# Optimization experiments

Hardware: AMD Instinct MI355X
Metric: run time of the kernel (lower is better)

Reference implementation:

```python
import jax, jax.numpy as jnp
import numpy as np

N_CAMS = 6
N_RAYS = 200
N_UNI = 32
N_G = 4
N_PG = 8
MAX_D = 100.0
SOM_SIG = 2.0
GRID_W = 400
RAW_W, RAW_H = 1600.0, 900.0
SCENE = np.array([-51.2, -51.2, -5.0, 51.2, 51.2, 3.0], dtype=np.float32)
LOSS_W = {'kl': 1.0, 'dist2closest': 0.01, 'color': 1.0, 'reprojection': 1.0}


def _pe(x):
    freqs = jnp.pi * (2.0 ** jnp.arange(6, dtype=x.dtype))
    xb = x[..., None, :] * freqs[:, None]
    flat = lambda t: t.reshape(t.shape[:-2] + (t.shape[-2] * t.shape[-1],))
    return jnp.concatenate([x, flat(jnp.sin(xb)), flat(jnp.cos(xb))], axis=-1)


def _bilinear(img, u, v):
    C, H, W = img.shape
    x0 = jnp.floor(u)
    y0 = jnp.floor(v)
    valid = (u >= 0) & (u <= W - 1) & (v >= 0) & (v <= H - 1)
    x0i = jnp.clip(x0.astype(jnp.int32), 0, W - 1)
    x1i = jnp.clip(x0i + 1, 0, W - 1)
    y0i = jnp.clip(y0.astype(jnp.int32), 0, H - 1)
    y1i = jnp.clip(y0i + 1, 0, H - 1)
    wx = u - x0
    wy = v - y0
    out = (img[:, y0i, x0i] * ((1 - wx) * (1 - wy))[None]
           + img[:, y0i, x1i] * (wx * (1 - wy))[None]
           + img[:, y1i, x0i] * ((1 - wx) * wy)[None]
           + img[:, y1i, x1i] * (wx * wy)[None])
    out = jnp.moveaxis(out, 0, -1) * valid[..., None]
    return out, valid


def _resnet_fc(feat, z, win, bin_, wz, bz, w0, b0, w1, b1, wout, bout):
    x = feat @ win + bin_
    for i in range(wz.shape[0]):
        x = x + z @ wz[i] + bz[i]
        h = jax.nn.relu(x)
        h = jax.nn.relu(h @ w0[i] + b0[i])
        h = h @ w1[i] + b1[i]
        x = x + h
    return jax.nn.relu(x) @ wout + bout


def _forward(cam_feat, bev_feat, source_imgs, target_imgs, raw_cam_Ks, source_cam_Ks,
             lidar2cams, source_cam2input_lidars, source_cam2target_cams,
             mlp_win, mlp_bin, mlp_wz, mlp_bz, mlp_w0, mlp_b0, mlp_w1, mlp_b1, mlp_wout, mlp_bout,
             g_win, g_bin, g_wz, g_bz, g_w0, g_b0, g_w1, g_b1, g_wout, g_bout, pixel_idx):
    cf = cam_feat[0]
    bf = bev_feat[0]
    si = source_imgs[0, 0]
    ti = target_imgs[0, 0]
    rK = raw_cam_Ks[0, :, :3, :3]
    sK = source_cam_Ks[0, 0, :, :3, :3]
    invK = jnp.linalg.inv(sK)
    l2c = lidar2cams[0]
    s2in = source_cam2input_lidars[0, 0]
    s2tg = source_cam2target_cams[0, 0]
    center = jnp.asarray((SCENE[:3] + SCENE[3:]) / 2.0)
    half = jnp.asarray((SCENE[3:] - SCENE[:3]) / 2.0)
    mlp_p = (mlp_win, mlp_bin, mlp_wz, mlp_bz, mlp_w0, mlp_b0, mlp_w1, mlp_b1, mlp_wout, mlp_bout)
    g_p = (g_win, g_bin, g_wz, g_bz, g_w0, g_b0, g_w1, g_b1, g_wout, g_bout)

    def per_cam(cf_c, si_c, ti_c, rK_c, sK_c, invK_c, l2c_c, s2in_c, s2tg_c, idx):
        N = idx.shape[0]
        x = (idx % GRID_W).astype(jnp.float32) * 2.0
        y = (idx // GRID_W).astype(jnp.float32) * 2.0
        pix_h = jnp.stack([x, y, jnp.ones_like(x)], axis=-1)
        dirs = pix_h @ invK_c.T
        d_u = (jnp.arange(N_UNI, dtype=jnp.float32) + 0.5) / N_UNI * MAX_D
        d_u_b = jnp.broadcast_to(d_u, (N, N_UNI))
        Hf, Wf = cf_c.shape[1], cf_c.shape[2]
        Hb, Wb = bf.shape[1], bf.shape[2]

        def eval_pts(d):
            pts_cam = dirs[:, None, :] * d[..., None]
            pts_lid = pts_cam @ s2in_c[:3, :3].T + s2in_c[:3, 3]
            pc = pts_lid @ l2c_c[:3, :3].T + l2c_c[:3, 3]
            z = pc[..., 2]
            zs = jnp.maximum(z, 1e-3)
            uvw = pc @ rK_c.T
            fu = uvw[..., 0] / zs * (Wf / RAW_W)
            fv = uvw[..., 1] / zs * (Hf / RAW_H)
            cam_lat, cval = _bilinear(cf_c, fu, fv)
            cval = cval & (z > 0.1)
            bx = (pts_lid[..., 0] - SCENE[0]) / (SCENE[3] - SCENE[0]) * (Wb - 1)
            by = (pts_lid[..., 1] - SCENE[1]) / (SCENE[4] - SCENE[1]) * (Hb - 1)
            bev_lat, bval = _bilinear(bf, bx, by)
            valid = cval & bval
            latent = jnp.concatenate([bev_lat, cam_lat], axis=-1) * valid[..., None]
            pln = (pts_lid - center) / half
            pcn = pts_cam / MAX_D
            vd = dirs / jnp.linalg.norm(dirs, axis=-1, keepdims=True)
            vdl = vd @ s2in_c[:3, :3].T
            vd_b = jnp.broadcast_to(vd[:, None, :], pcn.shape)
            vdl_b = jnp.broadcast_to(vdl[:, None, :], pcn.shape)
            feat = jnp.concatenate([_pe(pln), vdl_b, _pe(pcn), vd_b], axis=-1)
            return feat, latent, valid

        featc, latc, _valc = eval_pts(d_u_b)
        g = _resnet_fc(featc, latc, *g_p)
        logits = g[..., 0].reshape(N, N_G, N_PG)
        sval = g[..., 1].reshape(N, N_G, N_PG)
        wg = jax.nn.softmax(logits, axis=-1)
        d_grp = d_u.reshape(N_G, N_PG)
        mu = jnp.sum(wg * d_grp, axis=-1)
        std = jax.nn.softplus(jnp.sum(wg * sval, axis=-1)) + 0.1
        offs = jnp.linspace(-2.0, 2.0, N_PG)
        d_g = jnp.clip(mu[..., None] + std[..., None] * offs, 0.5, MAX_D).reshape(N, N_G * N_PG)
        d_all = jnp.sort(jnp.concatenate([d_u_b, d_g], axis=-1), axis=-1)

        featf, latf, valf = eval_pts(d_all)
        out = _resnet_fc(featf, latf, *mlp_p)
        rgb = jax.nn.sigmoid(out[..., :3])
        vf = valf.astype(jnp.float32)
        sigma = jax.nn.softplus(out[..., 3]) * vf
        delta = jnp.concatenate([d_all[..., 1:] - d_all[..., :-1],
                                 jnp.full((N, 1), 1e3, jnp.float32)], axis=-1)
        alpha = 1.0 - jnp.exp(-sigma * delta)
        trans = jnp.cumprod(1.0 - alpha + 1e-10, axis=-1)
        trans = jnp.concatenate([jnp.ones((N, 1), jnp.float32), trans[..., :-1]], axis=-1)
        w = alpha * trans
        color = jnp.sum(w[..., None] * rgb, axis=-2)
        depth = jnp.sum(w * d_all, axis=-1)
        rvr = vf.mean(axis=-1)

        dist2 = (d_all[:, None, :] - mu[:, :, None]) ** 2
        resp = jax.nn.softmax(-dist2 / (2.0 * SOM_SIG ** 2), axis=1)
        rw = resp * w[:, None, :] + 1e-8
        som_mean = jnp.sum(rw * d_all[:, None, :], axis=-1) / jnp.sum(rw, axis=-1)
        som_var = jnp.sum(rw * (d_all[:, None, :] - som_mean[..., None]) ** 2, axis=-1) / jnp.sum(rw, axis=-1)
        som_std = jnp.sqrt(som_var + 1e-6)
        kl = jnp.log(som_std / std) + (std ** 2 + (mu - som_mean) ** 2) / (2.0 * (som_var + 1e-6)) - 0.5
        loss_kl = kl.mean()

        dg = jnp.abs(mu - jax.lax.stop_gradient(depth)[:, None])
        loss_d2c = dg.min(axis=-1).mean()

        csrc, _ = _bilinear(si_c, x, y)
        loss_color = (jnp.abs(csrc - color) * rvr[:, None]).mean()

        pts_c = dirs * depth[:, None]
        pts_t = pts_c @ s2tg_c[:3, :3].T + s2tg_c[:3, 3]
        zt = jnp.maximum(pts_t[..., 2], 1e-3)
        uvt = pts_t @ sK_c.T
        pred, tval = _bilinear(ti_c, uvt[..., 0] / zt, uvt[..., 1] / zt)
        mask = (tval & (pts_t[..., 2] > 0.1) & (depth < 30.0)).astype(jnp.float32)
        l1 = jnp.abs(pred - csrc).mean(axis=-1)
        loss_re = jnp.sum(l1 * mask) / (jnp.sum(mask) + 1e-6)
        return loss_color, loss_kl, loss_d2c, loss_re

    lc, lkl, ld, lr = jax.vmap(per_cam)(cf, si, ti, rK, sK, invK, l2c, s2in, s2tg, pixel_idx)
    lr = jnp.where(jnp.isnan(lr), 0.0, lr)
    denom = float(N_CAMS)
    total = (LOSS_W['color'] * lc.sum() + LOSS_W['kl'] * lkl.sum()
             + LOSS_W['dist2closest'] * ld.sum() + LOSS_W['reprojection'] * lr.sum()) / denom
    return total


def setup_inputs() -> dict:
    key = jax.random.key(0)
    ks = jax.random.split(key, 8)
    f32 = jnp.float32
    cam_feat = jax.random.normal(ks[0], (1, 6, 256, 56, 100), f32)
    bev_feat = jax.random.normal(ks[1], (1, 512, 200, 200), f32)
    source_imgs = jax.random.uniform(ks[2], (1, 1, 6, 3, 300, 800), f32)
    target_imgs = jax.random.uniform(ks[3], (1, 1, 6, 3, 300, 800), f32)
    pixel_idx = jax.random.randint(ks[4], (6, N_RAYS), 0, GRID_W * 150)

    def rz(a):
        c, s = np.cos(a), np.sin(a)
        return np.array([[c, -s, 0.0], [s, c, 0.0], [0.0, 0.0, 1.0]], dtype=np.float32)
    A = np.array([[0, -1, 0], [0, 0, -1], [1, 0, 0]], dtype=np.float32)
    l2c = np.zeros((6, 4, 4), np.float32)
    for i in range(6):
        l2c[i, :3, :3] = A @ rz(-i * np.pi / 3)
        l2c[i, :3, 3] = np.array([0.0, 0.8, 0.5], np.float32)
        l2c[i, 3, 3] = 1.0
    s2in = np.linalg.inv(l2c).astype(np.float32)
    s2in[:, 0, 3] += 0.3
    s2tg = np.tile(np.eye(4, dtype=np.float32), (6, 1, 1))
    ang = 0.03
    s2tg[:, 0, 0] = np.cos(ang); s2tg[:, 0, 2] = np.sin(ang)
    s2tg[:, 2, 0] = -np.sin(ang); s2tg[:, 2, 2] = np.cos(ang)
    s2tg[:, 0, 3] = 0.3; s2tg[:, 2, 3] = 0.1
    rK = np.tile(np.eye(4, dtype=np.float32), (6, 1, 1))
    rK[:, 0, 0] = 800.0; rK[:, 1, 1] = 800.0; rK[:, 0, 2] = 800.0; rK[:, 1, 2] = 450.0
    sKm = np.tile(np.eye(4, dtype=np.float32), (6, 1, 1))
    sKm[:, 0, 0] = 400.0; sKm[:, 1, 1] = 400.0; sKm[:, 0, 2] = 400.0; sKm[:, 1, 2] = 150.0

    D_IN, D_H, D_LAT, NB = 84, 512, 768, 3

    def mk(k, dout):
        kk = jax.random.split(k, 5)
        return dict(
            win=jax.random.normal(kk[0], (D_IN, D_H), f32) * 0.1,
            bin=jnp.zeros((D_H,), f32),
            wz=jax.random.normal(kk[1], (NB, D_LAT, D_H), f32) * 0.036,
            bz=jnp.zeros((NB, D_H), f32),
            w0=jax.random.normal(kk[2], (NB, D_H, D_H), f32) * 0.044,
            b0=jnp.zeros((NB, D_H), f32),
            w1=jax.random.normal(kk[3], (NB, D_H, D_H), f32) * 0.044,
            b1=jnp.zeros((NB, D_H), f32),
            wout=jax.random.normal(kk[4], (D_H, dout), f32) * 0.044,
            bout=jnp.zeros((dout,), f32),
        )
    mp = mk(ks[5], 4)
    gp = mk(ks[6], 2)
    inp = {
        'cam_feat': cam_feat, 'bev_feat': bev_feat,
        'source_imgs': source_imgs, 'target_imgs': target_imgs,
        'raw_cam_Ks': jnp.asarray(rK)[None],
        'source_cam_Ks': jnp.asarray(sKm)[None, None],
        'lidar2cams': jnp.asarray(l2c)[None],
        'source_cam2input_lidars': jnp.asarray(s2in)[None, None],
        'source_cam2target_cams': jnp.asarray(s2tg)[None, None],
        'pixel_idx': pixel_idx,
    }
    for n, v in mp.items():
        inp['mlp_' + n] = v
    for n, v in gp.items():
        inp['g_' + n] = v
    return inp


def reference(cam_feat, bev_feat, source_imgs, target_imgs, raw_cam_Ks, source_cam_Ks,
              lidar2cams, source_cam2input_lidars, source_cam2target_cams,
              mlp_win, mlp_bin, mlp_wz, mlp_bz, mlp_w0, mlp_b0, mlp_w1, mlp_b1, mlp_wout, mlp_bout,
              g_win, g_bin, g_wz, g_bz, g_w0, g_b0, g_w1, g_b1, g_wout, g_bout, pixel_idx):
    return _forward(cam_feat, bev_feat, source_imgs, target_imgs, raw_cam_Ks, source_cam_Ks,
                    lidar2cams, source_cam2input_lidars, source_cam2target_cams,
                    mlp_win, mlp_bin, mlp_wz, mlp_bz, mlp_w0, mlp_b0, mlp_w1, mlp_b1, mlp_wout, mlp_bout,
                    g_win, g_bin, g_wz, g_bz, g_w0, g_b0, g_w1, g_b1, g_wout, g_bout, pixel_idx)
```

## Files before the change

kernel.cpp:

```cpp
#include <hip/hip_runtime.h>
#include <math.h>

typedef unsigned int uint32;
typedef short bf16x8 __attribute__((ext_vector_type(8)));
typedef float f32x4 __attribute__((ext_vector_type(4)));

__device__ __forceinline__ float sigmoidf_(float x){ return 1.0f/(1.0f+expf(-x)); }
__device__ __forceinline__ float softplusf_(float x){ return x>20.0f ? x : log1pf(expf(x)); }
__device__ __forceinline__ int iclampi(int v,int lo,int hi){ return v<lo?lo:(v>hi?hi:v); }

__device__ __forceinline__ float bf2f(uint32 u){ return __uint_as_float(u<<16); }
__device__ __forceinline__ unsigned short f2bf(float f){
  uint32 x = __float_as_uint(f);
  uint32 r = (x + 0x7fffu + ((x>>16)&1u)) >> 16;
  return (unsigned short)r;
}

typedef __attribute__((address_space(1))) const unsigned int ga_u32;
typedef __attribute__((address_space(3))) unsigned int ls_u32;
__device__ __forceinline__ void gl_lds16(const unsigned short* g, unsigned short* l){
  __builtin_amdgcn_global_load_lds((ga_u32*)g, (ls_u32*)l, 16, 0, 0);
}

__device__ __forceinline__ float pe_elem(int s, float vx, float vy, float vz){
  const float F0 = 3.14159265358979f;
  if (s < 3) return s==0?vx:(s==1?vy:vz);
  s -= 3;
  bool isCos = false;
  if (s >= 18){ s -= 18; isCos = true; }
  int fi = s/3, ci = s%3;
  float v = ci==0?vx:(ci==1?vy:vz);
  float f = F0 * (float)(1<<fi);
  return isCos ? cosf(f*v) : sinf(f*v);
}

__global__ __launch_bounds__(256) void transpose_cb_k(const float* __restrict__ in,
    unsigned short* __restrict__ out, int C, int S, int Cout,
    size_t inStride, size_t outStride, int rowStride)
{
  __shared__ float tile[32][33];
  int b = blockIdx.z;
  int s0 = blockIdx.x*32, c0 = blockIdx.y*32;
  int tx = threadIdx.x & 31, ty = threadIdx.x >> 5;
  #pragma unroll
  for (int i=0;i<32;i+=8){
    int c = c0+ty+i, s = s0+tx;
    tile[ty+i][tx] = (c<C && s<S) ? in[(size_t)b*inStride + (size_t)c*S + s] : 0.0f;
  }
  __syncthreads();
  #pragma unroll
  for (int i=0;i<32;i+=8){
    int s = s0+ty+i, c = c0+tx;
    if (s<S && c<Cout) out[(size_t)b*outStride + (size_t)s*rowStride + c] = f2bf(tile[tx][ty+i]);
  }
}

__global__ void combine_bias_k(const float* __restrict__ m_b1, const float* __restrict__ m_bz,
                               const float* __restrict__ g_b1, const float* __restrict__ g_bz,
                               const float* __restrict__ m_bin, const float* __restrict__ g_bin,
                               float* __restrict__ CB)
{
  int idx = blockIdx.x*blockDim.x + threadIdx.x;
  if (idx >= 3072) return;
  int w = idx >> 9, n = idx & 511;
  float v;
  if (w < 4){
    const float* b1 = (w < 2) ? m_b1 : g_b1;
    const float* bz = (w < 2) ? m_bz : g_bz;
    int i = w & 1;
    v = b1[i*512 + n] + bz[(i+1)*512 + n];
  } else if (w == 4) v = m_bin[n] + m_bz[n];
  else               v = g_bin[n] + g_bz[n];
  CB[idx] = v;
}

__global__ void setup_rays_k(const int* __restrict__ pix, const float* __restrict__ sK_all,
                             const float* __restrict__ s2in_all,
                             float* __restrict__ dirs, float* __restrict__ vd,
                             float* __restrict__ vdl)
{
  int r = blockIdx.x*blockDim.x + threadIdx.x;
  if (r >= 1200) return;
  int cam = r / 200;
  const float* sK = sK_all + cam*16;
  const float* s2in = s2in_all + cam*16;
  float a=sK[0],b=sK[1],c=sK[2],d=sK[4],e=sK[5],f=sK[6],g=sK[8],h=sK[9],i=sK[10];
  float det = a*(e*i-f*h) - b*(d*i-f*g) + c*(d*h-e*g);
  float inv00=(e*i-f*h)/det, inv01=(c*h-b*i)/det, inv02=(b*f-c*e)/det;
  float inv10=(f*g-d*i)/det, inv11=(a*i-c*g)/det, inv12=(c*d-a*f)/det;
  float inv20=(d*h-e*g)/det, inv21=(b*g-a*h)/det, inv22=(a*e-b*d)/det;
  int idx = pix[r];
  float x = (float)(idx % 400) * 2.0f;
  float y = (float)(idx / 400) * 2.0f;
  float dx = inv00*x + inv01*y + inv02;
  float dy = inv10*x + inv11*y + inv12;
  float dz = inv20*x + inv21*y + inv22;
  dirs[r*3+0]=dx; dirs[r*3+1]=dy; dirs[r*3+2]=dz;
  float n = sqrtf(dx*dx+dy*dy+dz*dz);
  float vx=dx/n, vy=dy/n, vz=dz/n;
  vd[r*3+0]=vx; vd[r*3+1]=vy; vd[r*3+2]=vz;
  vdl[r*3+0]=s2in[0]*vx + s2in[1]*vy + s2in[2]*vz;
  vdl[r*3+1]=s2in[4]*vx + s2in[5]*vy + s2in[6]*vz;
  vdl[r*3+2]=s2in[8]*vx + s2in[9]*vy + s2in[10]*vz;
}

__global__ __launch_bounds__(256) void eval2_k(
    const unsigned short* __restrict__ camT,
    const unsigned short* __restrict__ bevT,
    const float* __restrict__ dirs, const float* __restrict__ vd, const float* __restrict__ vdl,
    const float* __restrict__ dall, int ndepth, int R0,
    const float* __restrict__ s2in_all, const float* __restrict__ l2c_all, const float* __restrict__ rK_all,
    unsigned short* __restrict__ cat, float* __restrict__ vf)
{
  int p  = blockIdx.x;
  int rl = p / ndepth;
  int j  = p - rl*ndepth;
  int R  = R0 + rl;
  int cam = R / 200;
  const float* s2in = s2in_all + cam*16;
  const float* l2c  = l2c_all + cam*16;
  const float* rK   = rK_all + cam*16;
  float dx = dirs[R*3+0], dy = dirs[R*3+1], dz = dirs[R*3+2];
  float d = dall ? dall[(size_t)rl*ndepth + j] : (((float)j + 0.5f)/32.0f)*100.0f;
  float px = dx*d, py = dy*d, pz = dz*d;
  float lx = s2in[0]*px + s2in[1]*py + s2in[2]*pz + s2in[3];
  float ly = s2in[4]*px + s2in[5]*py + s2in[6]*pz + s2in[7];
  float lz = s2in[8]*px + s2in[9]*py + s2in[10]*pz + s2in[11];
  float ccx = l2c[0]*lx + l2c[1]*ly + l2c[2]*lz + l2c[3];
  float ccy = l2c[4]*lx + l2c[5]*ly + l2c[6]*lz + l2c[7];
  float ccz = l2c[8]*lx + l2c[9]*ly + l2c[10]*lz + l2c[11];
  float zs = fmaxf(ccz, 0.001f);
  float uu = rK[0]*ccx + rK[1]*ccy + rK[2]*ccz;
  float vv = rK[4]*ccx + rK[5]*ccy + rK[6]*ccz;
  float fu = uu/zs*(100.0f/1600.0f);
  float fv = vv/zs*(56.0f/900.0f);
  bool cvalid = (fu>=0.0f)&&(fu<=99.0f)&&(fv>=0.0f)&&(fv<=55.0f)&&(ccz>0.1f);
  float cfx0 = floorf(fu), cfy0 = floorf(fv);
  int cx0=iclampi((int)cfx0,0,99), cx1=iclampi(cx0+1,0,99);
  int cy0=iclampi((int)cfy0,0,55), cy1=iclampi(cy0+1,0,55);
  float cwx=fu-cfx0, cwy=fv-cfy0;
  float cw00=(1-cwx)*(1-cwy), cw01=cwx*(1-cwy), cw10=(1-cwx)*cwy, cw11=cwx*cwy;
  float bx = (lx+51.2f)/102.4f*199.0f;
  float by = (ly+51.2f)/102.4f*199.0f;
  bool bvalid = (bx>=0.0f)&&(bx<=199.0f)&&(by>=0.0f)&&(by<=199.0f);
  float bfx0=floorf(bx), bfy0=floorf(by);
  int bx0=iclampi((int)bfx0,0,199), bx1=iclampi(bx0+1,0,199);
  int by0=iclampi((int)bfy0,0,199), by1=iclampi(by0+1,0,199);
  float bwx=bx-bfx0, bwy=by-bfy0;
  float bw00=(1-bwx)*(1-bwy), bw01=bwx*(1-bwy), bw10=(1-bwx)*bwy, bw11=bwx*bwy;
  float vflag = (cvalid && bvalid) ? 1.0f : 0.0f;
  int t = threadIdx.x;
  uint32* catrow = (uint32*)(cat + (size_t)p*1408);
  {
    size_t sb00 = (size_t)(by0*200+bx0)*512, sb01 = (size_t)(by0*200+bx1)*512;
    size_t sb10 = (size_t)(by1*200+bx0)*512, sb11 = (size_t)(by1*200+bx1)*512;
    uint32 u00 = ((const uint32*)(bevT + sb00))[t];
    uint32 u01 = ((const uint32*)(bevT + sb01))[t];
    uint32 u10 = ((const uint32*)(bevT + sb10))[t];
    uint32 u11 = ((const uint32*)(bevT + sb11))[t];
    float lo = bw00*bf2f(u00&0xffffu) + bw01*bf2f(u01&0xffffu) + bw10*bf2f(u10&0xffffu) + bw11*bf2f(u11&0xffffu);
    float hi = bw00*bf2f(u00>>16) + bw01*bf2f(u01>>16) + bw10*bf2f(u10>>16) + bw11*bf2f(u11>>16);
    lo *= vflag; hi *= vflag;
    catrow[256 + t] = (uint32)f2bf(lo) | ((uint32)f2bf(hi)<<16);
  }
  if (t < 128){
    const unsigned short* cfT = camT + (size_t)cam*5600*256;
    size_t sc00 = (size_t)(cy0*100+cx0)*256, sc01 = (size_t)(cy0*100+cx1)*256;
    size_t sc10 = (size_t)(cy1*100+cx0)*256, sc11 = (size_t)(cy1*100+cx1)*256;
    uint32 u00 = ((const uint32*)(cfT + sc00))[t];
    uint32 u01 = ((const uint32*)(cfT + sc01))[t];
    uint32 u10 = ((const uint32*)(cfT + sc10))[t];
    uint32 u11 = ((const uint32*)(cfT + sc11))[t];
    float lo = cw00*bf2f(u00&0xffffu) + cw01*bf2f(u01&0xffffu) + cw10*bf2f(u10&0xffffu) + cw11*bf2f(u11&0xffffu);
    float hi = cw00*bf2f(u00>>16) + cw01*bf2f(u01>>16) + cw10*bf2f(u10>>16) + cw11*bf2f(u11>>16);
    lo *= vflag; hi *= vflag;
    catrow[512 + t] = (uint32)f2bf(lo) | ((uint32)f2bf(hi)<<16);
  }
  if (t < 64){
    float plx = lx/51.2f, ply = ly/51.2f, plz = (lz+1.0f)/4.0f;
    float pcx = px/100.0f, pcy = py/100.0f, pcz = pz/100.0f;
    float vx=vd[R*3], vy=vd[R*3+1], vz=vd[R*3+2];
    float wx=vdl[R*3], wy=vdl[R*3+1], wz=vdl[R*3+2];
    auto featv = [&](int s)->float{
      if (s >= 84) return 0.0f;
      if (s < 39)  return pe_elem(s, plx, ply, plz);
      if (s < 42)  return (s==39)?wx:((s==40)?wy:wz);
      if (s < 81)  return pe_elem(s-42, pcx, pcy, pcz);
      return (s==81)?vx:((s==82)?vy:vz);
    };
    float v0 = featv(2*t), v1 = featv(2*t+1);
    catrow[640 + t] = (uint32)f2bf(v0) | ((uint32)f2bf(v1)<<16);
  }
  if (vf && t==0) vf[p] = vflag;
}

#define GBM 128
#define GBN 128
#define GBK 64
template<int ACC, int RELU_OUT, int WRITE_XR>
__global__ __launch_bounds__(256) void mgemm_k(
    const unsigned short* __restrict__ A, int lda,
    const unsigned short* __restrict__ BT,
    const float* __restrict__ bias,
    unsigned short* __restrict__ C, int ldc,
    unsigned short* __restrict__ XR,
    int M, int N, int K)
{
  __shared__ unsigned short As[2][GBM*GBK];
  __shared__ unsigned short Bs[2][GBN*GBK];
  int w = blockIdx.x;
  int xcd = w & 7, ii = w >> 3;
  int colp = ii & 3, rgrp = ii >> 2;
  int rowp = rgrp*8 + xcd;
  int row0 = rowp*GBM, col0 = colp*GBN;
  if (row0 >= M) return;
  int tid = threadIdx.x;
  int lane = tid & 63, wave = tid >> 6;
  int wm = wave >> 1, wn = wave & 1;
  int l15 = lane & 15, l4 = lane >> 4;
  int lrow = lane >> 3;
  int lch  = lane & 7;
  int chsw = (lch ^ lrow) * 8;
  const unsigned short* aptr = A  + (size_t)(row0 + wave*32 + lrow)*lda + chsw;
  const unsigned short* bptr = BT + (size_t)(col0 + wave*32 + lrow)*K   + chsw;
  int woff = (wave*32)*64;

// ... 39 lines not shown
        #pragma unroll
        for (int nj=0;nj<4;++nj)
          acc[mi][nj] = __builtin_amdgcn_mfma_f32_16x16x32_bf16(a[mi], b[nj], acc[mi][nj], 0,0,0);
    }
  }
  #pragma unroll
  for (int mi=0;mi<4;++mi){
    int gr0 = row0 + wm*64 + mi*16 + l4*4;
    #pragma unroll
    for (int nj=0;nj<4;++nj){
      int gc = col0 + wn*64 + nj*16 + l15;
      if (gc >= N) continue;
      float bv = bias[gc];
      #pragma unroll
      for (int i=0;i<4;++i){
        int gr = gr0 + i;
        if (gr >= M) continue;
        float v = acc[mi][nj][i] + bv;
        if (ACC) v += bf2f((uint32)C[(size_t)gr*ldc + gc]);
        if (RELU_OUT) v = fmaxf(v, 0.0f);
        C[(size_t)gr*ldc + gc] = f2bf(v);
        if (WRITE_XR) XR[(size_t)gr*512 + gc] = f2bf(fmaxf(v, 0.0f));
      }
    }
  }
}

static inline int gemm_grid(int M){
  int nrow = (M + GBM - 1)/GBM;
  int nrowp = (nrow + 7) & ~7;
  return nrowp * 4;
}

__global__ __launch_bounds__(256) void outlayer_w_k(const unsigned short* __restrict__ X,
    const float* __restrict__ W, const float* __restrict__ b, float* __restrict__ O,
    int M, int dout)
{
  int wid = threadIdx.x >> 6, lane = threadIdx.x & 63;
  int row = blockIdx.x*4 + wid;
  if (row >= M) return;
  const unsigned short* xr = X + (size_t)row*512;
  float s[4] = {0,0,0,0};
  for (int k=lane; k<512; k+=64){
    float xv = fmaxf(bf2f((uint32)xr[k]), 0.0f);
    #pragma unroll
    for (int c=0;c<4;++c)
      if (c < dout) s[c] += xv * W[(size_t)k*dout + c];
  }
  #pragma unroll
  for (int c=0;c<4;++c)
    #pragma unroll
    for (int m=32;m;m>>=1) s[c] += __shfl_xor(s[c], m, 64);
  if (lane == 0)
    for (int c=0;c<dout;++c) O[(size_t)row*dout + c] = s[c] + b[c];
}

__global__ __launch_bounds__(256) void coarse_post_w_k(const float* __restrict__ OUTB,
    float* __restrict__ MU, float* __restrict__ STD, float* __restrict__ DALL,
    int R0, int rn)
{
  int wid = threadIdx.x >> 6, lane = threadIdx.x & 63;
  int rl = blockIdx.x*4 + wid;
  if (rl >= rn) return;
  int R = R0 + rl;
  float v = 0.0f, muv = 0.0f, sdv = 0.0f;
  if (lane < 32){
// ... 134 lines not shown
  for (int g=0;g<4;++g) mind = fminf(mind, fabsf(mu[g]-depth));
  const float* si = src_imgs + (size_t)cam*3*300*800;
  const float* ti = tgt_imgs + (size_t)cam*3*300*800;
  const float* s2tg = s2tg_all + cam*16;
  const float* sK = sK_all + cam*16;
  int idx = pix[R];
  float x = (float)(idx % 400) * 2.0f;
  float y = (float)(idx / 400) * 2.0f;
  float csrc[3]; bool sval;
  bilin_img(si, 300, 800, x, y, csrc, &sval);
  if (!sval){ csrc[0]=0; csrc[1]=0; csrc[2]=0; }
  float csum = fabsf(csrc[0]-c0)+fabsf(csrc[1]-c1)+fabsf(csrc[2]-c2);
  float dx=dirs[R*3], dy=dirs[R*3+1], dz=dirs[R*3+2];
  float px=dx*depth, py=dy*depth, pz=dz*depth;
  float tx=s2tg[0]*px+s2tg[1]*py+s2tg[2]*pz+s2tg[3];
  float ty=s2tg[4]*px+s2tg[5]*py+s2tg[6]*pz+s2tg[7];
  float tz=s2tg[8]*px+s2tg[9]*py+s2tg[10]*pz+s2tg[11];
  float zt=fmaxf(tz,0.001f);
  float uu=(sK[0]*tx+sK[1]*ty+sK[2]*tz)/zt;
  float vv=(sK[4]*tx+sK[5]*ty+sK[6]*tz)/zt;
  float pred[3]; bool tval;
  bilin_img(ti, 300, 800, uu, vv, pred, &tval);
  float tvf = tval?1.0f:0.0f;
  pred[0]*=tvf; pred[1]*=tvf; pred[2]*=tvf;
  float mask = (tval && (tz>0.1f) && (depth<30.0f)) ? 1.0f : 0.0f;
  float l1 = (fabsf(pred[0]-csrc[0])+fabsf(pred[1]-csrc[1])+fabsf(pred[2]-csrc[2]))*(1.0f/3.0f);
  float* a = acc + cam*8;
  atomicAdd(&a[0], csum*rvr);
  atomicAdd(&a[1], klsum);
  atomicAdd(&a[2], mind);
  atomicAdd(&a[3], l1*mask);
  atomicAdd(&a[4], mask);
}

__global__ void zero_acc_k(float* a){ a[threadIdx.x] = 0.0f; }

__global__ void finalize_k(const float* __restrict__ acc, float* __restrict__ out){
  if (threadIdx.x==0 && blockIdx.x==0){
    float tot = 0.0f;
    for (int c=0;c<6;++c){
      const float* a = acc + c*8;
      float lc  = a[0] / 600.0f;
      float lkl = a[1] / 800.0f;
      float ld  = a[2] / 200.0f;
      float lr  = a[3] / (a[4] + 1e-6f);
      if (lr != lr) lr = 0.0f;
      tot += lc + lkl + 0.01f*ld + lr;
    }
    out[0] = tot / 6.0f;
  }
}

static void run_mlp5(hipStream_t stream, int M,
   const unsigned short* WmT, const float* CBin,
   const unsigned short* W0T, const float* b0,
   const unsigned short* W1Wz, const float* CB,
   const unsigned short* W1T2, const float* b1,
   const float* wout, const float* bout, int dout,
   unsigned short* CAT, unsigned short* X, unsigned short* XR, float* OUTB)
{
  int g = gemm_grid(M);
  mgemm_k<0,0,1><<<g,256,0,stream>>>(CAT+512, 1408, WmT, CBin, X, 512, XR, M, 512, 896);
  for (int i=0;i<2;++i){
    mgemm_k<0,1,0><<<g,256,0,stream>>>(XR, 512, W0T + (size_t)i*512*512, b0 + i*512, CAT, 1408, nullptr, M, 512, 512);
    mgemm_k<1,0,1><<<g,256,0,stream>>>(CAT, 1408, W1Wz + (size_t)i*512*1280, CB + i*512, X, 512, XR, M, 512, 1280);
  }
  mgemm_k<0,1,0><<<g,256,0,stream>>>(XR, 512, W0T + (size_t)2*512*512, b0 + 2*512, CAT, 1408, nullptr, M, 512, 512);
  mgemm_k<1,0,0><<<g,256,0,stream>>>(CAT, 1408, W1T2, b1 + 2*512, X, 512, nullptr, M, 512, 512);
  outlayer_w_k<<<(M+3)/4, 256, 0, stream>>>(X, wout, bout, OUTB, M, dout);
}

extern "C" void kernel_launch(void* const* d_in, const int* in_sizes, int n_in,
                              void* d_out, int out_size, void* d_ws, size_t ws_size,
                              hipStream_t stream) {
  (void)in_sizes; (void)n_in; (void)out_size;
  const float* cam_feat = (const float*)d_in[0];
  const float* bev_feat = (const float*)d_in[1];
  const float* src_imgs = (const float*)d_in[2];
  const float* tgt_imgs = (const float*)d_in[3];
  const float* rK   = (const float*)d_in[4];
  const float* sK   = (const float*)d_in[5];
  const float* l2c  = (const float*)d_in[6];
  const float* s2in = (const float*)d_in[7];
  const float* s2tg = (const float*)d_in[8];
  const int*   pix  = (const int*)d_in[9];
  const float* mlp_win = (const float*)d_in[10];
  const float* mlp_bin = (const float*)d_in[11];
  const float* mlp_wz  = (const float*)d_in[12];
  const float* mlp_bz  = (const float*)d_in[13];
  const float* mlp_w0  = (const float*)d_in[14];
  const float* mlp_b0  = (const float*)d_in[15];
  const float* mlp_w1  = (const float*)d_in[16];
  const float* mlp_b1  = (const float*)d_in[17];
  const float* mlp_wout= (const float*)d_in[18];
  const float* mlp_bout= (const float*)d_in[19];
  const float* g_win = (const float*)d_in[20];
  const float* g_bin = (const float*)d_in[21];
  const float* g_wz  = (const float*)d_in[22];
  const float* g_bz  = (const float*)d_in[23];
  const float* g_w0  = (const float*)d_in[24];
  const float* g_b0  = (const float*)d_in[25];
// ... 5 lines not shown
  char* base = (char*)d_ws;
  size_t off = 0;
  auto alloc = [&](size_t bytes)->char*{
    char* p = base + off;
    off = (off + bytes + 255) & ~(size_t)255;
    return p;
  };
  float* ACC  = (float*)alloc(64*4);
  float* DIR  = (float*)alloc(3600*4);
  float* VD   = (float*)alloc(3600*4);
  float* VDL  = (float*)alloc(3600*4);
  float* MU   = (float*)alloc(4800*4);
  float* STD  = (float*)alloc(4800*4);
  float* CBm  = (float*)alloc(3072*4);
  unsigned short* bevT = (unsigned short*)alloc((size_t)40000*512*2);
  unsigned short* camT = (unsigned short*)alloc((size_t)6*5600*256*2);
  unsigned short* gWmT  = (unsigned short*)alloc((size_t)512*896*2);
  unsigned short* mWmT  = (unsigned short*)alloc((size_t)512*896*2);
  unsigned short* gW0T  = (unsigned short*)alloc((size_t)3*512*512*2);
  unsigned short* mW0T  = (unsigned short*)alloc((size_t)3*512*512*2);
  unsigned short* gW1Wz = (unsigned short*)alloc((size_t)2*512*1280*2);
  unsigned short* mW1Wz = (unsigned short*)alloc((size_t)2*512*1280*2);
  unsigned short* gW1T2 = (unsigned short*)alloc((size_t)512*512*2);
  unsigned short* mW1T2 = (unsigned short*)alloc((size_t)512*512*2);
  size_t fixed = off;
  const size_t perray = 256 + 180224 + 65536 + 65536 + 1024 + 256;
  const size_t SLACK = 512*1024;
  int Rc = 1200;
  {
    size_t need = fixed + (size_t)1200*perray + SLACK + 8192;
    if (need > ws_size){
      size_t avail = (ws_size > fixed + SLACK + 8192) ? (ws_size - fixed - SLACK - 8192) : perray;
      Rc = (int)(avail / perray);
      if (Rc < 2) Rc = 2;
      Rc &= ~1;
      if (Rc > 1200) Rc = 1200;
    }
  }
  float*          DALL = (float*)alloc((size_t)Rc*64*4);
  unsigned short* CAT  = (unsigned short*)alloc((size_t)Rc*64*1408*2);
  unsigned short* X    = (unsigned short*)alloc((size_t)Rc*64*512*2);
  unsigned short* XR   = (unsigned short*)alloc((size_t)Rc*64*512*2);
  float*          OUTB = (float*)alloc((size_t)Rc*64*4*4);
  float*          VF   = (float*)alloc((size_t)Rc*64*4);

  { dim3 g((40000+31)/32, (512+31)/32, 1);
    transpose_cb_k<<<g,256,0,stream>>>(bev_feat, bevT, 512, 40000, 512, 0, 0, 512); }
  { dim3 g((5600+31)/32, (256+31)/32, 6);
    transpose_cb_k<<<g,256,0,stream>>>(cam_feat, camT, 256, 5600, 256, (size_t)256*5600, (size_t)5600*256, 256); }
  { dim3 g((512+31)/32, (768+31)/32, 1);
    transpose_cb_k<<<g,256,0,stream>>>(g_wz,  gWmT, 768, 512, 768, 0, 0, 896);
    transpose_cb_k<<<g,256,0,stream>>>(mlp_wz, mWmT, 768, 512, 768, 0, 0, 896); }
  { dim3 g((512+31)/32, (128+31)/32, 1);
    transpose_cb_k<<<g,256,0,stream>>>(g_win,  gWmT+768, 84, 512, 128, 0, 0, 896);
    transpose_cb_k<<<g,256,0,stream>>>(mlp_win, mWmT+768, 84, 512, 128, 0, 0, 896); }
  { dim3 g((512+31)/32, (512+31)/32, 3);
    transpose_cb_k<<<g,256,0,stream>>>(g_w0,  gW0T, 512, 512, 512, (size_t)512*512, (size_t)512*512, 512);
    transpose_cb_k<<<g,256,0,stream>>>(mlp_w0, mW0T, 512, 512, 512, (size_t)512*512, (size_t)512*512, 512); }
  { dim3 g((512+31)/32, (512+31)/32, 2);
    transpose_cb_k<<<g,256,0,stream>>>(g_w1,  gW1Wz, 512, 512, 512, (size_t)512*512, (size_t)512*1280, 1280);
    transpose_cb_k<<<g,256,0,stream>>>(mlp_w1, mW1Wz, 512, 512, 512, (size_t)512*512, (size_t)512*1280, 1280); }
  { dim3 g((512+31)/32, (768+31)/32, 2);
    transpose_cb_k<<<g,256,0,stream>>>(g_wz + (size_t)768*512,  gW1Wz + 512, 768, 512, 768, (size_t)768*512, (size_t)512*1280, 1280);
    transpose_cb_k<<<g,256,0,stream>>>(mlp_wz + (size_t)768*512, mW1Wz + 512, 768, 512, 768, (size_t)768*512, (size_t)512*1280, 1280); }
  { dim3 g((512+31)/32, (512+31)/32, 1);
    transpose_cb_k<<<g,256,0,stream>>>(g_w1 + (size_t)2*512*512,  gW1T2, 512, 512, 512, 0, 0, 512);
    transpose_cb_k<<<g,256,0,stream>>>(mlp_w1 + (size_t)2*512*512, mW1T2, 512, 512, 512, 0, 0, 512); }
  combine_bias_k<<<12,256,0,stream>>>(mlp_b1, mlp_bz, g_b1, g_bz, mlp_bin, g_bin, CBm);

  zero_acc_k<<<1,64,0,stream>>>(ACC);
  setup_rays_k<<<5,256,0,stream>>>(pix, sK, s2in, DIR, VD, VDL);

  for (int R0=0; R0<1200; R0+=Rc){
    int rn = (1200 - R0 < Rc) ? (1200 - R0) : Rc;
    int Pc = rn*32;
    eval2_k<<<Pc,256,0,stream>>>(camT, bevT, DIR, VD, VDL,
        nullptr, 32, R0, s2in, l2c, rK, CAT, nullptr);
    run_mlp5(stream, Pc, gWmT, CBm+2560, gW0T, g_b0, gW1Wz, CBm+1024,
             gW1T2, g_b1, g_wout, g_bout, 2, CAT, X, XR, OUTB);
    coarse_post_w_k<<<(rn+3)/4,256,0,stream>>>(OUTB, MU, STD, DALL, R0, rn);
    int Pf = rn*64;
    eval2_k<<<Pf,256,0,stream>>>(camT, bevT, DIR, VD, VDL,
        DALL, 64, R0, s2in, l2c, rK, CAT, VF);
    run_mlp5(stream, Pf, mWmT, CBm+2048, mW0T, mlp_b0, mW1Wz, CBm,
             mW1T2, mlp_b1, mlp_wout, mlp_bout, 4, CAT, X, XR, OUTB);
    render_loss_w_k<<<(rn+3)/4,256,0,stream>>>(OUTB, VF, DALL, MU, STD,
        DIR, pix, src_imgs, tgt_imgs, s2tg, sK, ACC, R0, rn);
  }
  finalize_k<<<1,1,0,stream>>>(ACC, (float*)d_out);
}
```

Baseline: 2.121 ms.

## Add 256x256-tile 512-thread MFMA GEMM variant for large MLP batches

Adds a new bf16 MFMA GEMM kernel that uses 256x256 output tiles and 8 waves per block with double-buffered LDS staging through global_load_lds, plus XCD-aware block mapping. The MLP layers use it when M is a multiple of 256 and at least 65536; otherwise they fall back to the previous kernel. The larger tiles are meant to raise arithmetic intensity and reduce global re-reads of A and B. In exchange they need more LDS and registers per block, which lowers occupancy and leaves more padding waste. The ray-chunk size is now rounded to a multiple of 4 so that M=Rc*64 stays divisible by 256.

```diff
diff --git a/kernel.cpp b/kernel.cpp
--- a/kernel.cpp
+++ b/kernel.cpp
@@ -297,6 +297,104 @@
   return nrowp * 4;
 }
 
+template<int ACC, int RELU_OUT, int WRITE_XR>
+__global__ __launch_bounds__(512) void mgemm8_k(
+    const unsigned short* __restrict__ A, int lda,
+    const unsigned short* __restrict__ BT,
+    const float* __restrict__ bias,
+    unsigned short* __restrict__ C, int ldc,
+    unsigned short* __restrict__ XR,
+    int M, int N, int K)
+{
+  __shared__ unsigned short As[2][256*64];
+  __shared__ unsigned short Bs[2][256*64];
+  int w = blockIdx.x;
+  int xcd = w & 7, ii = w >> 3;
+  int colp = ii & 1, rgrp = ii >> 1;
+  int rowp = rgrp*8 + xcd;
+  int row0 = rowp*256, col0 = colp*256;
+  if (row0 >= M) return;
+  int tid = threadIdx.x;
+  int lane = tid & 63, wave = tid >> 6;
+  int wm = wave >> 2, wn = wave & 3;
+  int l15 = lane & 15, l4 = lane >> 4;
+  int lrow = lane >> 3, lch = lane & 7;
+  int chsw = (lch ^ lrow) * 8;
+  const unsigned short* aptr = A  + (size_t)(row0 + wave*32 + lrow)*lda + chsw;
+  const unsigned short* bptr = BT + (size_t)(col0 + wave*32 + lrow)*K   + chsw;
+  int woff = (wave*32)*64;
+
+  auto STAGE = [&](int buf, int kk){
+    unsigned short* ab = (buf ? &As[1][0] : &As[0][0]) + woff;
+    unsigned short* bb = (buf ? &Bs[1][0] : &Bs[0][0]) + woff;
+    #pragma unroll
+    for (int i=0;i<4;++i) gl_lds16(aptr + (size_t)i*8*lda + kk, ab + i*8*64);
+    #pragma unroll
+    for (int i=0;i<4;++i) gl_lds16(bptr + (size_t)i*8*K   + kk, bb + i*8*64);
+  };
+
+  f32x4 acc[8][4];
+  #pragma unroll
+  for (int mi=0;mi<8;++mi)
+    #pragma unroll
+    for (int nj=0;nj<4;++nj){ f32x4 z = {0.f,0.f,0.f,0.f}; acc[mi][nj] = z; }
+
+  STAGE(0, 0);
+  int nk = K / 64;
+  for (int t=0; t<nk; ++t){
+    __syncthreads();
+    if (t+1 < nk) STAGE((t+1)&1, (t+1)*64);
+    const unsigned short* Ab = (t&1) ? &As[1][0] : &As[0][0];
+    const unsigned short* Bb = (t&1) ? &Bs[1][0] : &Bs[0][0];
+    #pragma unroll
+    for (int ks=0; ks<2; ++ks){
+      bf16x8 a[8], b[4];
+      #pragma unroll
+      for (int mi=0;mi<8;++mi){
+        int row = wm*128 + mi*16 + l15;
+        int sc = (ks*4 + l4) ^ (row&7);
+        a[mi] = *(const bf16x8*)&Ab[row*64 + sc*8];
+      }
+      #pragma unroll
+      for (int nj=0;nj<4;++nj){
+        int colr = wn*64 + nj*16 + l15;
+        int sc = (ks*4 + l4) ^ (colr&7);
+        b[nj] = *(const bf16x8*)&Bb[colr*64 + sc*8];
+      }
+      #pragma unroll
+      for (int mi=0;mi<8;++mi)
+        #pragma unroll
+        for (int nj=0;nj<4;++nj)
+          acc[mi][nj] = __builtin_amdgcn_mfma_f32_16x16x32_bf16(a[mi], b[nj], acc[mi][nj], 0,0,0);
+    }
+  }
+  #pragma unroll
+  for (int mi=0;mi<8;++mi){
+    int gr0 = row0 + wm*128 + mi*16 + l4*4;
+    #pragma unroll
+    for (int nj=0;nj<4;++nj){
+      int gc = col0 + wn*64 + nj*16 + l15;
+      if (gc >= N) continue;
+      float bv = bias[gc];
+      #pragma unroll
+      for (int i=0;i<4;++i){
+        int gr = gr0 + i;
+        float v = acc[mi][nj][i] + bv;
+        if (ACC) v += bf2f((uint32)C[(size_t)gr*ldc + gc]);
+        if (RELU_OUT) v = fmaxf(v, 0.0f);
+        C[(size_t)gr*ldc + gc] = f2bf(v);
+        if (WRITE_XR) XR[(size_t)gr*512 + gc] = f2bf(fmaxf(v, 0.0f));
+      }
+    }
+  }
+}
+
+static inline int gemm8_grid(int M){
+  int nrow = (M + 255)/256;
+  int nrowp = (nrow + 7) & ~7;
+  return nrowp * 2;
+}
+
 __global__ __launch_bounds__(256) void outlayer_w_k(const unsigned short* __restrict__ X,
     const float* __restrict__ W, const float* __restrict__ b, float* __restrict__ O,
     int M, int dout)
@@ -516,6 +614,10 @@
   }
 }
 
+#define LAUNCH_GEMM(ACCv,RELUv,XRv, Aa,ldav, BTv, biasv, Cv,ldcv, XRp, Kv) \
+  do { if (use8) mgemm8_k<ACCv,RELUv,XRv><<<g8,512,0,stream>>>(Aa,ldav,BTv,biasv,Cv,ldcv,XRp,M,512,Kv); \
+       else      mgemm_k<ACCv,RELUv,XRv><<<g4,256,0,stream>>>(Aa,ldav,BTv,biasv,Cv,ldcv,XRp,M,512,Kv); } while(0)
+
 static void run_mlp5(hipStream_t stream, int M,
    const unsigned short* WmT, const float* CBin,
    const unsigned short* W0T, const float* b0,
@@ -524,14 +626,16 @@
    const float* wout, const float* bout, int dout,
    unsigned short* CAT, unsigned short* X, unsigned short* XR, float* OUTB)
 {
-  int g = gemm_grid(M);
-  mgemm_k<0,0,1><<<g,256,0,stream>>>(CAT+512, 1408, WmT, CBin, X, 512, XR, M, 512, 896);
+  bool use8 = (M % 256 == 0) && (M >= 65536);
+  int g4 = gemm_grid(M);
+  int g8 = gemm8_grid(M);
+  LAUNCH_GEMM(0,0,1, CAT+512,1408, WmT, CBin, X,512, XR, 896);
   for (int i=0;i<2;++i){
-    mgemm_k<0,1,0><<<g,256,0,stream>>>(XR, 512, W0T + (size_t)i*512*512, b0 + i*512, CAT, 1408, nullptr, M, 512, 512);
-    mgemm_k<1,0,1><<<g,256,0,stream>>>(CAT, 1408, W1Wz + (size_t)i*512*1280, CB + i*512, X, 512, XR, M, 512, 1280);
-  }
-  mgemm_k<0,1,0><<<g,256,0,stream>>>(XR, 512, W0T + (size_t)2*512*512, b0 + 2*512, CAT, 1408, nullptr, M, 512, 512);
-  mgemm_k<1,0,0><<<g,256,0,stream>>>(CAT, 1408, W1T2, b1 + 2*512, X, 512, nullptr, M, 512, 512);
+    LAUNCH_GEMM(0,1,0, XR,512, W0T + (size_t)i*512*512, b0 + i*512, CAT,1408, nullptr, 512);
+    LAUNCH_GEMM(1,0,1, CAT,1408, W1Wz + (size_t)i*512*1280, CB + i*512, X,512, XR, 1280);
+  }
+  LAUNCH_GEMM(0,1,0, XR,512, W0T + (size_t)2*512*512, b0 + 2*512, CAT,1408, nullptr, 512);
+  LAUNCH_GEMM(1,0,0, CAT,1408, W1T2, b1 + 2*512, X,512, nullptr, 512);
   outlayer_w_k<<<(M+3)/4, 256, 0, stream>>>(X, wout, bout, OUTB, M, dout);
 }
 
@@ -603,8 +707,8 @@
     if (need > ws_size){
       size_t avail = (ws_size > fixed + SLACK + 8192) ? (ws_size - fixed - SLACK - 8192) : perray;
       Rc = (int)(avail / perray);
-      if (Rc < 2) Rc = 2;
-      Rc &= ~1;
+      if (Rc < 4) Rc = 4;
+      Rc &= ~3;
       if (Rc > 1200) Rc = 1200;
     }
   }
```

Result: no change. 2.127 ms (+0.3%).

## Merge weight-prep launches and pack two samples per eval block

Applied to the files above, without the earlier changes.

The dozen weight-transpose and bias-combine launches become a single dispatch kernel, and accumulator zeroing folds into the ray setup kernel, cutting launch count. The feature-gather kernel now handles two sample points per 256-thread block, with each 128-thread half loading 8-byte vectors of BEV features. This halves the block count and widens the loads, at the cost of more complex per-block indexing. The chunk size is also rounded to a multiple of 4.

```diff
diff --git a/kernel.cpp b/kernel.cpp
--- a/kernel.cpp
+++ b/kernel.cpp
@@ -4,6 +4,7 @@
 typedef unsigned int uint32;
 typedef short bf16x8 __attribute__((ext_vector_type(8)));
 typedef float f32x4 __attribute__((ext_vector_type(4)));
+typedef uint32 u32x2 __attribute__((ext_vector_type(2)));
 
 __device__ __forceinline__ float sigmoidf_(float x){ return 1.0f/(1.0f+expf(-x)); }
 __device__ __forceinline__ float softplusf_(float x){ return x>20.0f ? x : log1pf(expf(x)); }
@@ -55,32 +56,77 @@
   }
 }
 
-__global__ void combine_bias_k(const float* __restrict__ m_b1, const float* __restrict__ m_bz,
-                               const float* __restrict__ g_b1, const float* __restrict__ g_bz,
-                               const float* __restrict__ m_bin, const float* __restrict__ g_bin,
-                               float* __restrict__ CB)
-{
-  int idx = blockIdx.x*blockDim.x + threadIdx.x;
-  if (idx >= 3072) return;
-  int w = idx >> 9, n = idx & 511;
-  float v;
-  if (w < 4){
-    const float* b1 = (w < 2) ? m_b1 : g_b1;
-    const float* bz = (w < 2) ? m_bz : g_bz;
-    int i = w & 1;
-    v = b1[i*512 + n] + bz[(i+1)*512 + n];
-  } else if (w == 4) v = m_bin[n] + m_bz[n];
-  else               v = g_bin[n] + g_bz[n];
-  CB[idx] = v;
+__global__ __launch_bounds__(256) void wprep_k(
+    const float* __restrict__ g_wz, const float* __restrict__ m_wz,
+    const float* __restrict__ g_win, const float* __restrict__ m_win,
+    const float* __restrict__ g_w0, const float* __restrict__ m_w0,
+    const float* __restrict__ g_w1, const float* __restrict__ m_w1,
+    unsigned short* gWmT, unsigned short* mWmT,
+    unsigned short* gW0T, unsigned short* mW0T,
+    unsigned short* gW1Wz, unsigned short* mW1Wz,
+    unsigned short* gW1T2, unsigned short* mW1T2,
+    const float* __restrict__ m_b1, const float* __restrict__ m_bz,
+    const float* __restrict__ g_b1, const float* __restrict__ g_bz,
+    const float* __restrict__ m_bin, const float* __restrict__ g_bin,
+    float* __restrict__ CB)
+{
+  __shared__ float tile[32][33];
+  int l = blockIdx.x;
+  const float* src; unsigned short* dst;
+  int C, Cout, rs, s_t, c_t;
+  if (l < 768){ int v=l/384, l2=l%384; s_t=l2%16; c_t=l2/16;
+    src = v? m_wz : g_wz; dst = v? mWmT : gWmT; C=768; Cout=768; rs=896; }
+  else if (l < 896){ int l0=l-768; int v=l0/64, l2=l0%64; s_t=l2%16; c_t=l2/16;
+    src = v? m_win : g_win; dst = (v? mWmT : gWmT) + 768; C=84; Cout=128; rs=896; }
+  else if (l < 2432){ int l0=l-896; int v=l0/768, l2=l0%768; int z=l2/256, l3=l2%256; s_t=l3%16; c_t=l3/16;
+    src = (v? m_w0 : g_w0) + (size_t)z*512*512; dst = (v? mW0T : gW0T) + (size_t)z*512*512;
+    C=512; Cout=512; rs=512; }
+  else if (l < 3456){ int l0=l-2432; int v=l0/512, l2=l0%512; int z=l2/256, l3=l2%256; s_t=l3%16; c_t=l3/16;
+    src = (v? m_w1 : g_w1) + (size_t)z*512*512; dst = (v? mW1Wz : gW1Wz) + (size_t)z*512*1280;
+    C=512; Cout=512; rs=1280; }
+  else if (l < 4992){ int l0=l-3456; int v=l0/768, l2=l0%768; int z=l2/384, l3=l2%384; s_t=l3%16; c_t=l3/16;
+    src = (v? m_wz : g_wz) + (size_t)(z+1)*768*512; dst = (v? mW1Wz : gW1Wz) + 512 + (size_t)z*512*1280;
+    C=768; Cout=768; rs=1280; }
+  else if (l < 5504){ int l0=l-4992; int v=l0/256, l2=l0%256; s_t=l2%16; c_t=l2/16;
+    src = (v? m_w1 : g_w1) + (size_t)2*512*512; dst = v? mW1T2 : gW1T2; C=512; Cout=512; rs=512; }
+  else {
+    int idx = (l-5504)*256 + threadIdx.x;
+    if (idx < 3072){
+      int w = idx >> 9, n = idx & 511;
+      float v;
+      if (w < 4){
+        const float* b1 = (w < 2) ? m_b1 : g_b1;
+        const float* bz = (w < 2) ? m_bz : g_bz;
+        int i = w & 1;
+        v = b1[i*512 + n] + bz[(i+1)*512 + n];
+      } else if (w == 4) v = m_bin[n] + m_bz[n];
+      else               v = g_bin[n] + g_bz[n];
+      CB[idx] = v;
+    }
+    return;
+  }
+  int s0 = s_t*32, c0 = c_t*32;
+  int tx = threadIdx.x & 31, ty = threadIdx.x >> 5;
+  #pragma unroll
+  for (int i=0;i<32;i+=8){
+    int c = c0+ty+i, s = s0+tx;
+    tile[ty+i][tx] = (c<C) ? src[(size_t)c*512 + s] : 0.0f;
+  }
+  __syncthreads();
+  #pragma unroll
+  for (int i=0;i<32;i+=8){
+    int s = s0+ty+i, c = c0+tx;
+    if (c<Cout) dst[(size_t)s*rs + c] = f2bf(tile[tx][ty+i]);
+  }
 }
 
 __global__ void setup_rays_k(const int* __restrict__ pix, const float* __restrict__ sK_all,
                              const float* __restrict__ s2in_all,
                              float* __restrict__ dirs, float* __restrict__ vd,
-                             float* __restrict__ vdl)
+                             float* __restrict__ vdl, float* __restrict__ acc)
 {
   int r = blockIdx.x*blockDim.x + threadIdx.x;
-  if (r >= 1200) return;
+  if (r >= 1200){ int z = r - 1200; if (z < 64) acc[z] = 0.0f; return; }
   int cam = r / 200;
   const float* sK = sK_all + cam*16;
   const float* s2in = s2in_all + cam*16;
@@ -108,11 +154,14 @@
     const unsigned short* __restrict__ camT,
     const unsigned short* __restrict__ bevT,
     const float* __restrict__ dirs, const float* __restrict__ vd, const float* __restrict__ vdl,
-    const float* __restrict__ dall, int ndepth, int R0,
+    const float* __restrict__ dall, int ndepth, int R0, int P,
     const float* __restrict__ s2in_all, const float* __restrict__ l2c_all, const float* __restrict__ rK_all,
     unsigned short* __restrict__ cat, float* __restrict__ vf)
 {
-  int p  = blockIdx.x;
+  int grp = threadIdx.x >> 7;
+  int tl  = threadIdx.x & 127;
+  int p = blockIdx.x*2 + grp;
+  if (p >= P) return;
   int rl = p / ndepth;
   int j  = p - rl*ndepth;
   int R  = R0 + rl;
@@ -149,34 +198,37 @@
   float bwx=bx-bfx0, bwy=by-bfy0;
   float bw00=(1-bwx)*(1-bwy), bw01=bwx*(1-bwy), bw10=(1-bwx)*bwy, bw11=bwx*bwy;
   float vflag = (cvalid && bvalid) ? 1.0f : 0.0f;
-  int t = threadIdx.x;
   uint32* catrow = (uint32*)(cat + (size_t)p*1408);
+  auto bil2 = [&](uint32 a, uint32 b, uint32 c, uint32 dd,
+                  float w00,float w01,float w10,float w11)->uint32{
+    float lo = w00*bf2f(a&0xffffu)+w01*bf2f(b&0xffffu)+w10*bf2f(c&0xffffu)+w11*bf2f(dd&0xffffu);
+    float hi = w00*bf2f(a>>16)+w01*bf2f(b>>16)+w10*bf2f(c>>16)+w11*bf2f(dd>>16);
+    lo *= vflag; hi *= vflag;
+    return (uint32)f2bf(lo) | ((uint32)f2bf(hi)<<16);
+  };
   {
     size_t sb00 = (size_t)(by0*200+bx0)*512, sb01 = (size_t)(by0*200+bx1)*512;
     size_t sb10 = (size_t)(by1*200+bx0)*512, sb11 = (size_t)(by1*200+bx1)*512;
-    uint32 u00 = ((const uint32*)(bevT + sb00))[t];
-    uint32 u01 = ((const uint32*)(bevT + sb01))[t];
-    uint32 u10 = ((const uint32*)(bevT + sb10))[t];
-    uint32 u11 = ((const uint32*)(bevT + sb11))[t];
-    float lo = bw00*bf2f(u00&0xffffu) + bw01*bf2f(u01&0xffffu) + bw10*bf2f(u10&0xffffu) + bw11*bf2f(u11&0xffffu);
-    float hi = bw00*bf2f(u00>>16) + bw01*bf2f(u01>>16) + bw10*bf2f(u10>>16) + bw11*bf2f(u11>>16);
-    lo *= vflag; hi *= vflag;
-    catrow[256 + t] = (uint32)f2bf(lo) | ((uint32)f2bf(hi)<<16);
-  }
-  if (t < 128){
+    u32x2 u00 = ((const u32x2*)(bevT + sb00))[tl];
+    u32x2 u01 = ((const u32x2*)(bevT + sb01))[tl];
+    u32x2 u10 = ((const u32x2*)(bevT + sb10))[tl];
+    u32x2 u11 = ((const u32x2*)(bevT + sb11))[tl];
+    u32x2 res;
+    res[0] = bil2(u00[0],u01[0],u10[0],u11[0], bw00,bw01,bw10,bw11);
+    res[1] = bil2(u00[1],u01[1],u10[1],u11[1], bw00,bw01,bw10,bw11);
+    ((u32x2*)catrow)[128 + tl] = res;
+  }
+  {
     const unsigned short* cfT = camT + (size_t)cam*5600*256;
     size_t sc00 = (size_t)(cy0*100+cx0)*256, sc01 = (size_t)(cy0*100+cx1)*256;
     size_t sc10 = (size_t)(cy1*100+cx0)*256, sc11 = (size_t)(cy1*100+cx1)*256;
-    uint32 u00 = ((const uint32*)(cfT + sc00))[t];
-    uint32 u01 = ((const uint32*)(cfT + sc01))[t];
-    uint32 u10 = ((const uint32*)(cfT + sc10))[t];
-    uint32 u11 = ((const uint32*)(cfT + sc11))[t];
-    float lo = cw00*bf2f(u00&0xffffu) + cw01*bf2f(u01&0xffffu) + cw10*bf2f(u10&0xffffu) + cw11*bf2f(u11&0xffffu);
-    float hi = cw00*bf2f(u00>>16) + cw01*bf2f(u01>>16) + cw10*bf2f(u10>>16) + cw11*bf2f(u11>>16);
-    lo *= vflag; hi *= vflag;
-    catrow[512 + t] = (uint32)f2bf(lo) | ((uint32)f2bf(hi)<<16);
-  }
-  if (t < 64){
+    uint32 u00 = ((const uint32*)(cfT + sc00))[tl];
+    uint32 u01 = ((const uint32*)(cfT + sc01))[tl];
+    uint32 u10 = ((const uint32*)(cfT + sc10))[tl];
+    uint32 u11 = ((const uint32*)(cfT + sc11))[tl];
+    catrow[512 + tl] = bil2(u00,u01,u10,u11, cw00,cw01,cw10,cw11);
+  }
+  if (tl < 64){
     float plx = lx/51.2f, ply = ly/51.2f, plz = (lz+1.0f)/4.0f;
     float pcx = px/100.0f, pcy = py/100.0f, pcz = pz/100.0f;
     float vx=vd[R*3], vy=vd[R*3+1], vz=vd[R*3+2];
@@ -188,10 +240,10 @@
       if (s < 81)  return pe_elem(s-42, pcx, pcy, pcz);
       return (s==81)?vx:((s==82)?vy:vz);
     };
-    float v0 = featv(2*t), v1 = featv(2*t+1);
-    catrow[640 + t] = (uint32)f2bf(v0) | ((uint32)f2bf(v1)<<16);
-  }
-  if (vf && t==0) vf[p] = vflag;
+    float v0 = featv(2*tl), v1 = featv(2*tl+1);
+    catrow[640 + tl] = (uint32)f2bf(v0) | ((uint32)f2bf(v1)<<16);
+  }
+  if (vf && tl==0) vf[p] = vflag;
 }
 
 #define GBM 128
@@ -497,8 +549,6 @@
   atomicAdd(&a[3], l1*mask);
   atomicAdd(&a[4], mask);
 }
-
-__global__ void zero_acc_k(float* a){ a[threadIdx.x] = 0.0f; }
 
 __global__ void finalize_k(const float* __restrict__ acc, float* __restrict__ out){
   if (threadIdx.x==0 && blockIdx.x==0){
@@ -603,8 +653,8 @@
     if (need > ws_size){
       size_t avail = (ws_size > fixed + SLACK + 8192) ? (ws_size - fixed - SLACK - 8192) : perray;
       Rc = (int)(avail / perray);
-      if (Rc < 2) Rc = 2;
-      Rc &= ~1;
+      if (Rc < 4) Rc = 4;
+      Rc &= ~3;
       if (Rc > 1200) Rc = 1200;
     }
   }
@@ -619,40 +669,24 @@
     transpose_cb_k<<<g,256,0,stream>>>(bev_feat, bevT, 512, 40000, 512, 0, 0, 512); }
   { dim3 g((5600+31)/32, (256+31)/32, 6);
     transpose_cb_k<<<g,256,0,stream>>>(cam_feat, camT, 256, 5600, 256, (size_t)256*5600, (size_t)5600*256, 256); }
-  { dim3 g((512+31)/32, (768+31)/32, 1);
-    transpose_cb_k<<<g,256,0,stream>>>(g_wz,  gWmT, 768, 512, 768, 0, 0, 896);
-    transpose_cb_k<<<g,256,0,stream>>>(mlp_wz, mWmT, 768, 512, 768, 0, 0, 896); }
-  { dim3 g((512+31)/32, (128+31)/32, 1);
-    transpose_cb_k<<<g,256,0,stream>>>(g_win,  gWmT+768, 84, 512, 128, 0, 0, 896);
-    transpose_cb_k<<<g,256,0,stream>>>(mlp_win, mWmT+768, 84, 512, 128, 0, 0, 896); }
-  { dim3 g((512+31)/32, (512+31)/32, 3);
-    transpose_cb_k<<<g,256,0,stream>>>(g_w0,  gW0T, 512, 512, 512, (size_t)512*512, (size_t)512*512, 512);
-    transpose_cb_k<<<g,256,0,stream>>>(mlp_w0, mW0T, 512, 512, 512, (size_t)512*512, (size_t)512*512, 512); }
-  { dim3 g((512+31)/32, (512+31)/32, 2);
-    transpose_cb_k<<<g,256,0,stream>>>(g_w1,  gW1Wz, 512, 512, 512, (size_t)512*512, (size_t)512*1280, 1280);
-    transpose_cb_k<<<g,256,0,stream>>>(mlp_w1, mW1Wz, 512, 512, 512, (size_t)512*512, (size_t)512*1280, 1280); }
-  { dim3 g((512+31)/32, (768+31)/32, 2);
-    transpose_cb_k<<<g,256,0,stream>>>(g_wz + (size_t)768*512,  gW1Wz + 512, 768, 512, 768, (size_t)768*512, (size_t)512*1280, 1280);
-    transpose_cb_k<<<g,256,0,stream>>>(mlp_wz + (size_t)768*512, mW1Wz + 512, 768, 512, 768, (size_t)768*512, (size_t)512*1280, 1280); }
-  { dim3 g((512+31)/32, (512+31)/32, 1);
-    transpose_cb_k<<<g,256,0,stream>>>(g_w1 + (size_t)2*512*512,  gW1T2, 512, 512, 512, 0, 0, 512);
-    transpose_cb_k<<<g,256,0,stream>>>(mlp_w1 + (size_t)2*512*512, mW1T2, 512, 512, 512, 0, 0, 512); }
-  combine_bias_k<<<12,256,0,stream>>>(mlp_b1, mlp_bz, g_b1, g_bz, mlp_bin, g_bin, CBm);
-
-  zero_acc_k<<<1,64,0,stream>>>(ACC);
-  setup_rays_k<<<5,256,0,stream>>>(pix, sK, s2in, DIR, VD, VDL);
+  wprep_k<<<5516,256,0,stream>>>(
+      g_wz, mlp_wz, g_win, mlp_win, g_w0, mlp_w0, g_w1, mlp_w1,
+      gWmT, mWmT, gW0T, mW0T, gW1Wz, mW1Wz, gW1T2, mW1T2,
+      mlp_b1, mlp_bz, g_b1, g_bz, mlp_bin, g_bin, CBm);
+
+  setup_rays_k<<<5,256,0,stream>>>(pix, sK, s2in, DIR, VD, VDL, ACC);
 
   for (int R0=0; R0<1200; R0+=Rc){
     int rn = (1200 - R0 < Rc) ? (1200 - R0) : Rc;
     int Pc = rn*32;
-    eval2_k<<<Pc,256,0,stream>>>(camT, bevT, DIR, VD, VDL,
-        nullptr, 32, R0, s2in, l2c, rK, CAT, nullptr);
+    eval2_k<<<(Pc+1)/2,256,0,stream>>>(camT, bevT, DIR, VD, VDL,
+        nullptr, 32, R0, Pc, s2in, l2c, rK, CAT, nullptr);
     run_mlp5(stream, Pc, gWmT, CBm+2560, gW0T, g_b0, gW1Wz, CBm+1024,
              gW1T2, g_b1, g_wout, g_bout, 2, CAT, X, XR, OUTB);
     coarse_post_w_k<<<(rn+3)/4,256,0,stream>>>(OUTB, MU, STD, DALL, R0, rn);
     int Pf = rn*64;
-    eval2_k<<<Pf,256,0,stream>>>(camT, bevT, DIR, VD, VDL,
-        DALL, 64, R0, s2in, l2c, rK, CAT, VF);
+    eval2_k<<<(Pf+1)/2,256,0,stream>>>(camT, bevT, DIR, VD, VDL,
+        DALL, 64, R0, Pf, s2in, l2c, rK, CAT, VF);
     run_mlp5(stream, Pf, mWmT, CBm+2048, mW0T, mlp_b0, mW1Wz, CBm,
              mW1T2, mlp_b1, mlp_wout, mlp_bout, 4, CAT, X, XR, OUTB);
     render_loss_w_k<<<(rn+3)/4,256,0,stream>>>(OUTB, VF, DALL, MU, STD,
```

After: 2.043 ms, median of 2. -3.7%, faster.
